# Kernel optimization log

Measured on AMD Instinct MI355X. Metric: run time of the kernel, lower is better.

Reference implementation:

```python
import jax, jax.numpy as jnp
import numpy as np

BATCH, SEQ, EMBED, HIDDEN, VOCAB = 32, 64, 512, 512, 32000

def setup_inputs() -> dict:
    key = jax.random.key(0)
    ks = jax.random.split(key, 11)
    s = lambda k, shape, scale: jax.random.normal(k, shape, dtype=jnp.float32) * scale
    return {
        "features": s(ks[0], (BATCH, HIDDEN), 1.0),
        "captions": jax.random.randint(ks[1], (BATCH, SEQ), 0, VOCAB),
        "embedding": s(ks[2], (VOCAB, EMBED), 1.0),
        "Wz_w": s(ks[3], (HIDDEN, EMBED + HIDDEN), 0.03),
        "Wz_b": s(ks[4], (HIDDEN,), 0.03),
        "Wr_w": s(ks[5], (HIDDEN, EMBED + HIDDEN), 0.03),
        "Wr_b": s(ks[6], (HIDDEN,), 0.03),
        "Wh_w": s(ks[7], (HIDDEN, EMBED + HIDDEN), 0.03),
        "Wh_b": s(ks[8], (HIDDEN,), 0.03),
        "fc_w": s(ks[9], (VOCAB, HIDDEN), 0.03),
        "fc_b": s(ks[10], (VOCAB,), 0.03),
    }

def reference(features, captions, embedding, Wz_w, Wz_b, Wr_w, Wr_b, Wh_w, Wh_b, fc_w, fc_b):
    # embeddings: [B, T, E] -> scan over time with xs [T, B, E]
    emb = embedding[captions]                      # [B, T, E]
    xs = jnp.swapaxes(emb, 0, 1)                   # [T, B, E]

    def step(h, x_t):
        comb = jnp.concatenate([x_t, h], axis=1)                   # [B, E+H]
        z = jax.nn.sigmoid(comb @ Wz_w.T + Wz_b)                   # update gate
        r = jax.nn.sigmoid(comb @ Wr_w.T + Wr_b)                   # reset gate
        comb_r = jnp.concatenate([x_t, r * h], axis=1)
        h_tilde = jnp.tanh(comb_r @ Wh_w.T + Wh_b)
        h_new = (1.0 - z) * h + z * h_tilde
        return h_new, h_new

    _, hs = jax.lax.scan(step, features, xs)       # hs: [T, B, H]
    hs = jnp.swapaxes(hs, 0, 1)                    # [B, T, H]
    # output projection done once over all timesteps (same math as per-step fc_out)
    logits = jnp.einsum('bth,vh->btv', hs, fc_w) + fc_b  # [B, T, V]
    return logits
```

## Files before the change

kernel.cpp:

```cpp
#include <hip/hip_runtime.h>
#include <hip/hip_bf16.h>

typedef __bf16 bf16;
typedef __bf16 bf16x8 __attribute__((ext_vector_type(8)));
typedef float f32x4 __attribute__((ext_vector_type(4)));
typedef unsigned int u32x4 __attribute__((ext_vector_type(4)));

#define B_SZ 32
#define T_SZ 64
#define H_SZ 512
#define V_SZ 32000
#define NWG_REC 8

__device__ __forceinline__ float sigmoidf_(float v) { return 1.0f / (1.0f + expf(-v)); }

__device__ __forceinline__ bf16x8 cvt8(const float* __restrict__ p) {
  float4 a = *(const float4*)p;
  float4 b = *(const float4*)(p + 4);
  bf16x8 o;
  o[0] = (bf16)a.x; o[1] = (bf16)a.y; o[2] = (bf16)a.z; o[3] = (bf16)a.w;
  o[4] = (bf16)b.x; o[5] = (bf16)b.y; o[6] = (bf16)b.z; o[7] = (bf16)b.w;
  return o;
}

__device__ __forceinline__ u32x4 llc_load8(const bf16* p) {
  u32x4 r;
  asm volatile("global_load_dwordx4 %0, %1, off sc0 sc1" : "=v"(r) : "v"(p));
  return r;
}
__device__ __forceinline__ void llc_store_bf16(bf16* p, float v) {
  unsigned short us = __builtin_bit_cast(unsigned short, (bf16)v);
  unsigned int w = us;
  asm volatile("global_store_short %0, %1, off sc0 sc1" :: "v"(p), "v"(w) : "memory");
}

__global__ void init_k(const float* __restrict__ feat, bf16* __restrict__ h_g,
                       int* __restrict__ ctr) {
  int i = blockIdx.x * blockDim.x + threadIdx.x;
  if (i < B_SZ * H_SZ) h_g[i] = (bf16)feat[i];
  if (i == 0) *ctr = 0;
}

__global__ void cvt_fcw(const float* __restrict__ src, bf16* __restrict__ dst, long n) {
  long i = (long)(blockIdx.x * blockDim.x + threadIdx.x) * 8;
  if (i < n) *(bf16x8*)(dst + i) = cvt8(src + i);
}

__global__ void cvt_wh(const float* __restrict__ Wz, const float* __restrict__ Wr,
                       const float* __restrict__ Wh, bf16* __restrict__ dst) {
  int i = blockIdx.x * blockDim.x + threadIdx.x;
  int w = i >> 15;
  int rem = i & 32767;
  int n = rem >> 6;
  int k8 = (rem & 63) * 8;
  const float* W = (w == 0) ? Wz : (w == 1) ? Wr : Wh;
  *(bf16x8*)(dst + (long)w * 262144 + n * 512 + k8) = cvt8(W + (long)n * 1024 + 512 + k8);
}

template<int AMODE, bool BF32>
__global__ __launch_bounds__(256) void gemm_bt(
    const void* __restrict__ Av,
    const int* __restrict__ caps, const float* __restrict__ emb,
    const void* __restrict__ Bv, int ldb,
    const float* __restrict__ bias,
    float* __restrict__ C, long ldc,
    int K, int mtiles)
{
  __shared__ __align__(16) bf16 lA[128 * 32];
  __shared__ __align__(16) bf16 lB[128 * 32];
  const int tid  = threadIdx.x;
  const int lane = tid & 63;
  const int l15  = lane & 15;
  const int kb8  = (lane >> 4) * 8;
  const int wid  = tid >> 6;
  const int wm   = wid >> 1, wn = wid & 1;
  const int wg   = blockIdx.x;
  const int mtile = wg % mtiles, ntile = wg / mtiles;
  const int m0 = mtile * 128, n0 = ntile * 128;

  f32x4 acc[4][4] = {};

  for (int k0 = 0; k0 < K; k0 += 32) {
    #pragma unroll
    for (int j = 0; j < 2; ++j) {
      int c = j * 256 + tid;
      int row = c >> 2;
      int kc = (c & 3) * 8;
      bf16x8 av;
      if (AMODE == 1) av = cvt8(emb + (long)caps[m0 + row] * K + k0 + kc);
      else            av = *(const bf16x8*)((const bf16*)Av + (long)(m0 + row) * K + k0 + kc);
      *(bf16x8*)&lA[row * 32 + kc] = av;
      bf16x8 bv;
      if (BF32) bv = cvt8((const float*)Bv + (long)(n0 + row) * ldb + k0 + kc);
      else      bv = *(const bf16x8*)((const bf16*)Bv + (long)(n0 + row) * ldb + k0 + kc);
      *(bf16x8*)&lB[row * 32 + kc] = bv;
    }
    __syncthreads();
    bf16x8 af[4], bfr[4];
    #pragma unroll
    for (int mf = 0; mf < 4; ++mf)
      af[mf] = *(const bf16x8*)&lA[(wm * 64 + mf * 16 + l15) * 32 + kb8];
    #pragma unroll
    for (int nf = 0; nf < 4; ++nf)
      bfr[nf] = *(const bf16x8*)&lB[(wn * 64 + nf * 16 + l15) * 32 + kb8];
    #pragma unroll
    for (int mf = 0; mf < 4; ++mf)
      #pragma unroll
      for (int nf = 0; nf < 4; ++nf)
        acc[mf][nf] = __builtin_amdgcn_mfma_f32_16x16x32_bf16(af[mf], bfr[nf], acc[mf][nf], 0, 0, 0);
    __syncthreads();
  }

  #pragma unroll
  for (int mf = 0; mf < 4; ++mf)
    #pragma unroll
    for (int nf = 0; nf < 4; ++nf)
      #pragma unroll
      for (int r = 0; r < 4; ++r) {
        int row = m0 + wm * 64 + mf * 16 + (lane >> 4) * 4 + r;
        int col = n0 + wn * 64 + nf * 16 + l15;
        C[(long)row * ldc + col] = acc[mf][nf][r] + bias[col];
      }
}

__device__ __forceinline__ void gridbar(int* ctr, int target) {
  asm volatile("s_waitcnt vmcnt(0) lgkmcnt(0)" ::: "memory");
  __syncthreads();
  if (threadIdx.x == 0) {
    __hip_atomic_fetch_add(ctr, 1, __ATOMIC_RELAXED, __HIP_MEMORY_SCOPE_AGENT);
    while (__hip_atomic_load(ctr, __ATOMIC_RELAXED, __HIP_MEMORY_SCOPE_AGENT) < target)
      __builtin_amdgcn_s_sleep(1);
  }
  __syncthreads();
}

__global__ __launch_bounds__(512, 2) void gru_rec(
    const float* __restrict__ X,
    const bf16* __restrict__ Wzh, const bf16* __restrict__ Wrh, const bf16* __restrict__ Whh,
    const float* __restrict__ feat,
    bf16* __restrict__ h_g, bf16* __restrict__ rh_g,
    bf16* __restrict__ hs, int* ctr)
{
  __shared__ __align__(16) char ldsb[16384];
  const int tid  = threadIdx.x;
  const int u    = blockIdx.x * 8 + (tid >> 6);
  const int lane = tid & 63;
  const int l15  = lane & 15;
  const int kb   = (lane >> 4) * 8;
  const int rq   = (lane >> 4) * 4;
  const int b0   = (u >> 5) * 16;
  const int c0   = (u & 31) * 16;
  const int gcol = c0 + l15;

  u32x4 Bz[16], Br[16], Bh[16];
  #pragma unroll
  for (int kk = 0; kk < 16; ++kk) {
    Bz[kk] = *(const u32x4*)(Wzh + (long)gcol * 512 + kk * 32 + kb);
    Br[kk] = *(const u32x4*)(Wrh + (long)gcol * 512 + kk * 32 + kb);
    Bh[kk] = *(const u32x4*)(Whh + (long)gcol * 512 + kk * 32 + kb);
  }
  #pragma unroll
  for (int kk = 0; kk < 16; ++kk)
    asm volatile("" : "+v"(Bz[kk]), "+v"(Br[kk]), "+v"(Bh[kk]));

  float hprev[4];
  #pragma unroll
  for (int r = 0; r < 4; ++r) hprev[r] = feat[(b0 + rq + r) * 512 + gcol];

  int xrow[4];
  #pragma unroll
  for (int r = 0; r < 4; ++r) xrow[r] = (b0 + rq + r) * 64 * 1536;

  float xz[4], xr[4];
  #pragma unroll
  for (int r = 0; r < 4; ++r) {
    xz[r] = X[xrow[r] + gcol];
    xr[r] = X[xrow[r] + 512 + gcol];
  }

  const int srow0 = tid >> 6;
  const int soff0 = (tid * 16) ^ ((srow0 & 7) << 4);
  const int soff1 = (8192 + tid * 16) ^ ((srow0 & 7) << 4);
  const int fbase = (l15 * 1024 + (lane >> 4) * 16) ^ ((l15 & 7) << 4);

  int epoch = 0;
  for (int t = 0; t < T_SZ; ++t) {
    {
      const bf16* src = h_g + b0 * 512;
      u32x4 v0 = llc_load8(src + tid * 8);
      u32x4 v1 = llc_load8(src + 4096 + tid * 8);
      asm volatile("s_waitcnt vmcnt(0)" ::: "memory");
      __builtin_amdgcn_sched_barrier(0);
      *(u32x4*)(ldsb + soff0) = v0;
      *(u32x4*)(ldsb + soff1) = v1;
    }
    __syncthreads();
    f32x4 ze = {}, re = {};
    #pragma unroll
    for (int kk = 0; kk < 16; ++kk) {
      bf16x8 a = *(const bf16x8*)(ldsb + (fbase ^ (kk * 64)));
      ze = __builtin_amdgcn_mfma_f32_16x16x32_bf16(a, __builtin_bit_cast(bf16x8, Bz[kk]), ze, 0, 0, 0);
      re = __builtin_amdgcn_mfma_f32_16x16x32_bf16(a, __builtin_bit_cast(bf16x8, Br[kk]), re, 0, 0, 0);
    }
    float xh[4];
    #pragma unroll
    for (int r = 0; r < 4; ++r) xh[r] = X[xrow[r] + t * 1536 + 1024 + gcol];
    f32x4 zf;
    #pragma unroll
    for (int r = 0; r < 4; ++r) {
      zf[r] = sigmoidf_(ze[r] + xz[r]);
      float rv = sigmoidf_(re[r] + xr[r]);
      llc_store_bf16(rh_g + (b0 + rq + r) * 512 + gcol, rv * hprev[r]);
    }
    ++epoch;
    gridbar(ctr, NWG_REC * epoch);

    {
      const bf16* src = rh_g + b0 * 512;
      u32x4 v0 = llc_load8(src + tid * 8);
      u32x4 v1 = llc_load8(src + 4096 + tid * 8);
      asm volatile("s_waitcnt vmcnt(0)" ::: "memory");
      __builtin_amdgcn_sched_barrier(0);
      *(u32x4*)(ldsb + soff0) = v0;
      *(u32x4*)(ldsb + soff1) = v1;
    }
    __syncthreads();
    f32x4 he = {};
    #pragma unroll
    for (int kk = 0; kk < 16; ++kk) {
      bf16x8 a = *(const bf16x8*)(ldsb + (fbase ^ (kk * 64)));
      he = __builtin_amdgcn_mfma_f32_16x16x32_bf16(a, __builtin_bit_cast(bf16x8, Bh[kk]), he, 0, 0, 0);
    }
    if (t + 1 < T_SZ) {
      #pragma unroll
      for (int r = 0; r < 4; ++r) {
        xz[r] = X[xrow[r] + (t + 1) * 1536 + gcol];
        xr[r] = X[xrow[r] + (t + 1) * 1536 + 512 + gcol];
      }
    }
    #pragma unroll
    for (int r = 0; r < 4; ++r) {
      int b = b0 + rq + r;
      float ht = tanhf(he[r] + xh[r]);
      float hn = hprev[r] + zf[r] * (ht - hprev[r]);
      hprev[r] = hn;
      llc_store_bf16(h_g + b * 512 + gcol, hn);
      hs[(long)(b * 64 + t) * 512 + gcol] = (bf16)hn;
    }
    ++epoch;
    gridbar(ctr, NWG_REC * epoch);
  }
}

extern "C" void kernel_launch(void* const* d_in, const int* in_sizes, int n_in,
                              void* d_out, int out_size, void* d_ws, size_t ws_size,
                              hipStream_t stream) {
  const float* feat = (const float*)d_in[0];
  const int*   caps = (const int*)d_in[1];
  const float* emb  = (const float*)d_in[2];
  const float* Wz_w = (const float*)d_in[3];
  const float* Wz_b = (const float*)d_in[4];
  const float* Wr_w = (const float*)d_in[5];
  const float* Wr_b = (const float*)d_in[6];
  const float* Wh_w = (const float*)d_in[7];
  const float* Wh_b = (const float*)d_in[8];
  const float* fc_w = (const float*)d_in[9];
  const float* fc_b = (const float*)d_in[10];
  float* out = (float*)d_out;

  char* ws = (char*)d_ws;
  float* X_all = (float*)(ws + 0);
  bf16*  h_g   = (bf16*) (ws + 12582912);
  bf16*  rh_g  = (bf16*) (ws + 12615680);
  bf16*  hs    = (bf16*) (ws + 12648448);
  bf16*  Whp   = (bf16*) (ws + 14745600);
  int*   ctr   = (int*)  (ws + 16318464);
  bf16*  fcw16 = (bf16*) (ws + 16318528);
  const bool cvt_fc = (ws_size >= (size_t)49086600);

  init_k<<<dim3(64), dim3(256), 0, stream>>>(feat, h_g, ctr);
  cvt_wh<<<dim3(384), dim3(256), 0, stream>>>(Wz_w, Wr_w, Wh_w, Whp);
  if (cvt_fc)
    cvt_fcw<<<dim3(8000), dim3(256), 0, stream>>>(fc_w, fcw16, (long)V_SZ * H_SZ);

  gemm_bt<1, true><<<dim3(64), dim3(256), 0, stream>>>(
      nullptr, caps, emb, Wz_w, 1024, Wz_b, X_all + 0,    1536, 512, 16);
  gemm_bt<1, true><<<dim3(64), dim3(256), 0, stream>>>(
      nullptr, caps, emb, Wr_w, 1024, Wr_b, X_all + 512,  1536, 512, 16);
  gemm_bt<1, true><<<dim3(64), dim3(256), 0, stream>>>(
      nullptr, caps, emb, Wh_w, 1024, Wh_b, X_all + 1024, 1536, 512, 16);

  gru_rec<<<dim3(NWG_REC), dim3(512), 0, stream>>>(
      X_all, Whp, Whp + 262144, Whp + 524288, feat, h_g, rh_g, hs, ctr);

  if (cvt_fc)
    gemm_bt<0, false><<<dim3(4000), dim3(256), 0, stream>>>(
        hs, nullptr, nullptr, fcw16, 512, fc_b, out, 32000, 512, 16);
  else
    gemm_bt<0, true><<<dim3(4000), dim3(256), 0, stream>>>(
        hs, nullptr, nullptr, fc_w, 512, fc_b, out, 32000, 512, 16);
}
```

Baseline: 734.8 us.

## Split recurrence sync per batch group, overlap fc weight conversion, merge launches

The recurrent kernel now syncs only the 4 workgroups that share a batch group, using a per-group counter polled per wavefront instead of a grid-wide barrier. The h and rh operands are loaded straight from L2 into registers, skipping the LDS staging. Wh is streamed from memory each step instead of held in registers, which frees registers at the cost of extra loads. The fc_w bf16 conversion runs on 56 extra workgroups alongside the recurrence, and the three input-projection GEMMs and the prep kernels are each merged into a single launch. The aim is to cut barrier latency and launch count, and to hide the conversion behind the serial recurrence.

Result: slower. 1.250 ms (+70.1%).

```diff
diff --git a/kernel.cpp b/kernel.cpp
--- a/kernel.cpp
+++ b/kernel.cpp
@@ -11,6 +11,7 @@
 #define H_SZ 512
 #define V_SZ 32000
 #define NWG_REC 8
+#define NWG_TOT 64
 
 __device__ __forceinline__ float sigmoidf_(float v) { return 1.0f / (1.0f + expf(-v)); }
 
@@ -23,30 +24,32 @@
   return o;
 }
 
-__device__ __forceinline__ u32x4 llc_load8(const bf16* p) {
-  u32x4 r;
-  asm volatile("global_load_dwordx4 %0, %1, off sc0 sc1" : "=v"(r) : "v"(p));
+#define GLD(dst, base, off) \
+  asm volatile("global_load_dwordx4 %0, %1, off offset:" off " sc0 sc1" \
+               : "=v"(dst) : "v"(base))
+#define LOADALL(af, base) do { \
+  GLD(af[0],  base, "0");   GLD(af[1],  base, "64");  GLD(af[2],  base, "128"); GLD(af[3],  base, "192"); \
+  GLD(af[4],  base, "256"); GLD(af[5],  base, "320"); GLD(af[6],  base, "384"); GLD(af[7],  base, "448"); \
+  GLD(af[8],  base, "512"); GLD(af[9],  base, "576"); GLD(af[10], base, "640"); GLD(af[11], base, "704"); \
+  GLD(af[12], base, "768"); GLD(af[13], base, "832"); GLD(af[14], base, "896"); GLD(af[15], base, "960"); \
+} while (0)
+
+#define GST2(base, off, val) do { \
+  unsigned int w_ = (unsigned int)__builtin_bit_cast(unsigned short, (bf16)(val)); \
+  asm volatile("global_store_short %0, %1, off offset:" off " sc0 sc1" \
+               :: "v"(base), "v"(w_) : "memory"); \
+} while (0)
+
+__device__ __forceinline__ int llc_poll(const int* p) {
+  int r;
+  asm volatile("global_load_dword %0, %1, off sc0 sc1\n\ts_waitcnt vmcnt(0)"
+               : "=v"(r) : "v"(p) : "memory");
   return r;
 }
-__device__ __forceinline__ void llc_store_bf16(bf16* p, float v) {
-  unsigned short us = __builtin_bit_cast(unsigned short, (bf16)v);
-  unsigned int w = us;
-  asm volatile("global_store_short %0, %1, off sc0 sc1" :: "v"(p), "v"(w) : "memory");
-}
-
-__global__ void init_k(const float* __restrict__ feat, bf16* __restrict__ h_g,
-                       int* __restrict__ ctr) {
-  int i = blockIdx.x * blockDim.x + threadIdx.x;
-  if (i < B_SZ * H_SZ) h_g[i] = (bf16)feat[i];
-  if (i == 0) *ctr = 0;
-}
-
-__global__ void cvt_fcw(const float* __restrict__ src, bf16* __restrict__ dst, long n) {
-  long i = (long)(blockIdx.x * blockDim.x + threadIdx.x) * 8;
-  if (i < n) *(bf16x8*)(dst + i) = cvt8(src + i);
-}
-
-__global__ void cvt_wh(const float* __restrict__ Wz, const float* __restrict__ Wr,
+
+__global__ void prep_k(const float* __restrict__ feat, bf16* __restrict__ h_g,
+                       int* __restrict__ ctr,
+                       const float* __restrict__ Wz, const float* __restrict__ Wr,
                        const float* __restrict__ Wh, bf16* __restrict__ dst) {
   int i = blockIdx.x * blockDim.x + threadIdx.x;
   int w = i >> 15;
@@ -55,16 +58,16 @@
   int k8 = (rem & 63) * 8;
   const float* W = (w == 0) ? Wz : (w == 1) ? Wr : Wh;
   *(bf16x8*)(dst + (long)w * 262144 + n * 512 + k8) = cvt8(W + (long)n * 1024 + 512 + k8);
+  if (i < B_SZ * H_SZ) h_g[i] = (bf16)feat[i];
+  if (i == 0) { ctr[0] = 0; ctr[64] = 0; }
 }
 
 template<int AMODE, bool BF32>
 __global__ __launch_bounds__(256) void gemm_bt(
-    const void* __restrict__ Av,
-    const int* __restrict__ caps, const float* __restrict__ emb,
-    const void* __restrict__ Bv, int ldb,
-    const float* __restrict__ bias,
-    float* __restrict__ C, long ldc,
-    int K, int mtiles)
+    const void* __restrict__ Av, const int* __restrict__ caps, const float* __restrict__ emb,
+    const void* __restrict__ B0, const void* __restrict__ B1, const void* __restrict__ B2, int ldb,
+    const float* __restrict__ bias0, const float* __restrict__ bias1, const float* __restrict__ bias2,
+    float* __restrict__ C, long ldc, int K, int mtiles)
 {
   __shared__ __align__(16) bf16 lA[128 * 32];
   __shared__ __align__(16) bf16 lB[128 * 32];
@@ -78,6 +81,14 @@
   const int mtile = wg % mtiles, ntile = wg / mtiles;
   const int m0 = mtile * 128, n0 = ntile * 128;
 
+  const void* Bv; const float* bias; int nb;
+  if (AMODE == 1) {
+    int wsel = n0 >> 9;
+    Bv = wsel == 0 ? B0 : wsel == 1 ? B1 : B2;
+    bias = wsel == 0 ? bias0 : wsel == 1 ? bias1 : bias2;
+    nb = n0 & 511;
+  } else { Bv = B0; bias = bias0; nb = n0; }
+
   f32x4 acc[4][4] = {};
 
   for (int k0 = 0; k0 < K; k0 += 32) {
@@ -91,8 +102,8 @@
       else            av = *(const bf16x8*)((const bf16*)Av + (long)(m0 + row) * K + k0 + kc);
       *(bf16x8*)&lA[row * 32 + kc] = av;
       bf16x8 bv;
-      if (BF32) bv = cvt8((const float*)Bv + (long)(n0 + row) * ldb + k0 + kc);
-      else      bv = *(const bf16x8*)((const bf16*)Bv + (long)(n0 + row) * ldb + k0 + kc);
+      if (BF32) bv = cvt8((const float*)Bv + (long)(nb + row) * ldb + k0 + kc);
+      else      bv = *(const bf16x8*)((const bf16*)Bv + (long)(nb + row) * ldb + k0 + kc);
       *(bf16x8*)&lB[row * 32 + kc] = bv;
     }
     __syncthreads();
@@ -118,20 +129,9 @@
       #pragma unroll
       for (int r = 0; r < 4; ++r) {
         int row = m0 + wm * 64 + mf * 16 + (lane >> 4) * 4 + r;
-        int col = n0 + wn * 64 + nf * 16 + l15;
-        C[(long)row * ldc + col] = acc[mf][nf][r] + bias[col];
+        int lc  = wn * 64 + nf * 16 + l15;
+        C[(long)row * ldc + n0 + lc] = acc[mf][nf][r] + bias[nb + lc];
       }
-}
-
-__device__ __forceinline__ void gridbar(int* ctr, int target) {
-  asm volatile("s_waitcnt vmcnt(0) lgkmcnt(0)" ::: "memory");
-  __syncthreads();
-  if (threadIdx.x == 0) {
-    __hip_atomic_fetch_add(ctr, 1, __ATOMIC_RELAXED, __HIP_MEMORY_SCOPE_AGENT);
-    while (__hip_atomic_load(ctr, __ATOMIC_RELAXED, __HIP_MEMORY_SCOPE_AGENT) < target)
-      __builtin_amdgcn_s_sleep(1);
-  }
-  __syncthreads();
 }
 
 __global__ __launch_bounds__(512, 2) void gru_rec(
@@ -139,116 +139,127 @@
     const bf16* __restrict__ Wzh, const bf16* __restrict__ Wrh, const bf16* __restrict__ Whh,
     const float* __restrict__ feat,
     bf16* __restrict__ h_g, bf16* __restrict__ rh_g,
-    bf16* __restrict__ hs, int* ctr)
+    bf16* __restrict__ hs, int* __restrict__ ctr,
+    const float* __restrict__ fcw_src, bf16* __restrict__ fcw_dst, int do_cvt)
 {
-  __shared__ __align__(16) char ldsb[16384];
-  const int tid  = threadIdx.x;
+  const int tid = threadIdx.x;
+  if (blockIdx.x >= NWG_REC) {
+    if (do_cvt) {
+      long base = ((long)(blockIdx.x - NWG_REC) * 512 + tid) * 8;
+      const long stride = (long)(NWG_TOT - NWG_REC) * 512 * 8;
+      for (long i = base; i < (long)V_SZ * H_SZ; i += stride)
+        *(bf16x8*)(fcw_dst + i) = cvt8(fcw_src + i);
+    }
+    return;
+  }
+
+  const int lane = tid & 63;
   const int u    = blockIdx.x * 8 + (tid >> 6);
-  const int lane = tid & 63;
   const int l15  = lane & 15;
   const int kb   = (lane >> 4) * 8;
   const int rq   = (lane >> 4) * 4;
-  const int b0   = (u >> 5) * 16;
-  const int c0   = (u & 31) * 16;
-  const int gcol = c0 + l15;
-
-  u32x4 Bz[16], Br[16], Bh[16];
+  const int grp  = u >> 5;
+  const int b0   = grp * 16;
+  const int gcol = (u & 31) * 16 + l15;
+  int* mctr = ctr + grp * 64;
+
+  u32x4 Bz[16], Br[16];
   #pragma unroll
   for (int kk = 0; kk < 16; ++kk) {
     Bz[kk] = *(const u32x4*)(Wzh + (long)gcol * 512 + kk * 32 + kb);
     Br[kk] = *(const u32x4*)(Wrh + (long)gcol * 512 + kk * 32 + kb);
-    Bh[kk] = *(const u32x4*)(Whh + (long)gcol * 512 + kk * 32 + kb);
-  }
-  #pragma unroll
-  for (int kk = 0; kk < 16; ++kk)
-    asm volatile("" : "+v"(Bz[kk]), "+v"(Br[kk]), "+v"(Bh[kk]));
+  }
+  const bf16* whbase = Whh + (long)gcol * 512 + kb;
 
   float hprev[4];
   #pragma unroll
   for (int r = 0; r < 4; ++r) hprev[r] = feat[(b0 + rq + r) * 512 + gcol];
 
-  int xrow[4];
-  #pragma unroll
-  for (int r = 0; r < 4; ++r) xrow[r] = (b0 + rq + r) * 64 * 1536;
-
+  const float* xb = X + (long)(b0 + rq) * 64 * 1536 + gcol;
   float xz[4], xr[4];
   #pragma unroll
   for (int r = 0; r < 4; ++r) {
-    xz[r] = X[xrow[r] + gcol];
-    xr[r] = X[xrow[r] + 512 + gcol];
-  }
-
-  const int srow0 = tid >> 6;
-  const int soff0 = (tid * 16) ^ ((srow0 & 7) << 4);
-  const int soff1 = (8192 + tid * 16) ^ ((srow0 & 7) << 4);
-  const int fbase = (l15 * 1024 + (lane >> 4) * 16) ^ ((l15 & 7) << 4);
-
-  int epoch = 0;
+    xz[r] = xb[r * 98304];
+    xr[r] = xb[r * 98304 + 512];
+  }
+
+  const bf16* ah   = h_g  + (b0 + l15) * 512 + kb;
+  const bf16* arh  = rh_g + (b0 + l15) * 512 + kb;
+  bf16* rhst = rh_g + (b0 + rq) * 512 + gcol;
+  bf16* hst  = h_g  + (b0 + rq) * 512 + gcol;
+  bf16* hsst = hs + (long)(b0 + rq) * 64 * 512 + gcol;
+
+  int tgt = 0;
   for (int t = 0; t < T_SZ; ++t) {
+    u32x4 af[16];
+    LOADALL(af, ah);
+    asm volatile("s_waitcnt vmcnt(0)" ::: "memory");
+    __builtin_amdgcn_sched_barrier(0);
+    f32x4 ze = {}, re = {};
+    #pragma unroll
+    for (int kk = 0; kk < 16; ++kk) {
+      bf16x8 a = __builtin_bit_cast(bf16x8, af[kk]);
+      ze = __builtin_amdgcn_mfma_f32_16x16x32_bf16(a, __builtin_bit_cast(bf16x8, Bz[kk]), ze, 0, 0, 0);
+      re = __builtin_amdgcn_mfma_f32_16x16x32_bf16(a, __builtin_bit_cast(bf16x8, Br[kk]), re, 0, 0, 0);
+    }
+    f32x4 zf;
     {
-      const bf16* src = h_g + b0 * 512;
-      u32x4 v0 = llc_load8(src + tid * 8);
-      u32x4 v1 = llc_load8(src + 4096 + tid * 8);
+      float r0 = sigmoidf_(re[0] + xr[0]) * hprev[0];
+      float r1 = sigmoidf_(re[1] + xr[1]) * hprev[1];
+      float r2 = sigmoidf_(re[2] + xr[2]) * hprev[2];
+      float r3 = sigmoidf_(re[3] + xr[3]) * hprev[3];
+      GST2(rhst, "0", r0); GST2(rhst, "1024", r1); GST2(rhst, "2048", r2); GST2(rhst, "3072", r3);
+      #pragma unroll
+      for (int r = 0; r < 4; ++r) zf[r] = sigmoidf_(ze[r] + xz[r]);
+    }
+    asm volatile("s_waitcnt vmcnt(0)" ::: "memory");
+    __builtin_amdgcn_sched_barrier(0);
+    tgt += 32;
+    if (lane == 0) __hip_atomic_fetch_add(mctr, 1, __ATOMIC_RELAXED, __HIP_MEMORY_SCOPE_AGENT);
+    __builtin_amdgcn_sched_barrier(0);
+    while (llc_poll(mctr) < tgt) __builtin_amdgcn_s_sleep(1);
+    __builtin_amdgcn_sched_barrier(0);
+
+    LOADALL(af, arh);
+    float xh[4];
+    #pragma unroll
+    for (int r = 0; r < 4; ++r) xh[r] = xb[r * 98304 + t * 1536 + 1024];
+    asm volatile("s_waitcnt vmcnt(0)" ::: "memory");
+    __builtin_amdgcn_sched_barrier(0);
+    f32x4 he = {};
+    #pragma unroll
+    for (int kk = 0; kk < 16; ++kk) {
+      u32x4 bh = *(const u32x4*)(whbase + kk * 32);
+      he = __builtin_amdgcn_mfma_f32_16x16x32_bf16(
+          __builtin_bit_cast(bf16x8, af[kk]), __builtin_bit_cast(bf16x8, bh), he, 0, 0, 0);
+    }
+    #pragma unroll
+    for (int r = 0; r < 4; ++r) {
+      float ht = tanhf(he[r] + xh[r]);
+      hprev[r] = hprev[r] + zf[r] * (ht - hprev[r]);
+    }
+    GST2(hst, "0", hprev[0]); GST2(hst, "1024", hprev[1]);
+    GST2(hst, "2048", hprev[2]); GST2(hst, "3072", hprev[3]);
+
+    if (t + 1 < T_SZ) {
       asm volatile("s_waitcnt vmcnt(0)" ::: "memory");
       __builtin_amdgcn_sched_barrier(0);
-      *(u32x4*)(ldsb + soff0) = v0;
-      *(u32x4*)(ldsb + soff1) = v1;
-    }
-    __syncthreads();
-    f32x4 ze = {}, re = {};
-    #pragma unroll
-    for (int kk = 0; kk < 16; ++kk) {
-      bf16x8 a = *(const bf16x8*)(ldsb + (fbase ^ (kk * 64)));
-      ze = __builtin_amdgcn_mfma_f32_16x16x32_bf16(a, __builtin_bit_cast(bf16x8, Bz[kk]), ze, 0, 0, 0);
-      re = __builtin_amdgcn_mfma_f32_16x16x32_bf16(a, __builtin_bit_cast(bf16x8, Br[kk]), re, 0, 0, 0);
-    }
-    float xh[4];
-    #pragma unroll
-    for (int r = 0; r < 4; ++r) xh[r] = X[xrow[r] + t * 1536 + 1024 + gcol];
-    f32x4 zf;
-    #pragma unroll
-    for (int r = 0; r < 4; ++r) {
-      zf[r] = sigmoidf_(ze[r] + xz[r]);
-      float rv = sigmoidf_(re[r] + xr[r]);
-      llc_store_bf16(rh_g + (b0 + rq + r) * 512 + gcol, rv * hprev[r]);
-    }
-    ++epoch;
-    gridbar(ctr, NWG_REC * epoch);
-
-    {
-      const bf16* src = rh_g + b0 * 512;
-      u32x4 v0 = llc_load8(src + tid * 8);
-      u32x4 v1 = llc_load8(src + 4096 + tid * 8);
-      asm volatile("s_waitcnt vmcnt(0)" ::: "memory");
+      tgt += 32;
+      if (lane == 0) __hip_atomic_fetch_add(mctr, 1, __ATOMIC_RELAXED, __HIP_MEMORY_SCOPE_AGENT);
+      #pragma unroll
+      for (int r = 0; r < 4; ++r) hsst[r * 32768 + t * 512] = (bf16)hprev[r];
+      #pragma unroll
+      for (int r = 0; r < 4; ++r) {
+        xz[r] = xb[r * 98304 + (t + 1) * 1536];
+        xr[r] = xb[r * 98304 + (t + 1) * 1536 + 512];
+      }
       __builtin_amdgcn_sched_barrier(0);
-      *(u32x4*)(ldsb + soff0) = v0;
-      *(u32x4*)(ldsb + soff1) = v1;
-    }
-    __syncthreads();
-    f32x4 he = {};
-    #pragma unroll
-    for (int kk = 0; kk < 16; ++kk) {
-      bf16x8 a = *(const bf16x8*)(ldsb + (fbase ^ (kk * 64)));
-      he = __builtin_amdgcn_mfma_f32_16x16x32_bf16(a, __builtin_bit_cast(bf16x8, Bh[kk]), he, 0, 0, 0);
-    }
-    if (t + 1 < T_SZ) {
-      #pragma unroll
-      for (int r = 0; r < 4; ++r) {
-        xz[r] = X[xrow[r] + (t + 1) * 1536 + gcol];
-        xr[r] = X[xrow[r] + (t + 1) * 1536 + 512 + gcol];
-      }
-    }
-    #pragma unroll
-    for (int r = 0; r < 4; ++r) {
-      int b = b0 + rq + r;
-      float ht = tanhf(he[r] + xh[r]);
-      float hn = hprev[r] + zf[r] * (ht - hprev[r]);
-      hprev[r] = hn;
-      llc_store_bf16(h_g + b * 512 + gcol, hn);
-      hs[(long)(b * 64 + t) * 512 + gcol] = (bf16)hn;
-    }
-    ++epoch;
-    gridbar(ctr, NWG_REC * epoch);
+      while (llc_poll(mctr) < tgt) __builtin_amdgcn_s_sleep(1);
+      __builtin_amdgcn_sched_barrier(0);
+    } else {
+      #pragma unroll
+      for (int r = 0; r < 4; ++r) hsst[r * 32768 + t * 512] = (bf16)hprev[r];
+    }
   }
 }
 
@@ -275,28 +286,25 @@
   bf16*  hs    = (bf16*) (ws + 12648448);
   bf16*  Whp   = (bf16*) (ws + 14745600);
   int*   ctr   = (int*)  (ws + 16318464);
-  bf16*  fcw16 = (bf16*) (ws + 16318528);
-  const bool cvt_fc = (ws_size >= (size_t)49086600);
-
-  init_k<<<dim3(64), dim3(256), 0, stream>>>(feat, h_g, ctr);
-  cvt_wh<<<dim3(384), dim3(256), 0, stream>>>(Wz_w, Wr_w, Wh_w, Whp);
-  if (cvt_fc)
-    cvt_fcw<<<dim3(8000), dim3(256), 0, stream>>>(fc_w, fcw16, (long)V_SZ * H_SZ);
-
-  gemm_bt<1, true><<<dim3(64), dim3(256), 0, stream>>>(
-      nullptr, caps, emb, Wz_w, 1024, Wz_b, X_all + 0,    1536, 512, 16);
-  gemm_bt<1, true><<<dim3(64), dim3(256), 0, stream>>>(
-      nullptr, caps, emb, Wr_w, 1024, Wr_b, X_all + 512,  1536, 512, 16);
-  gemm_bt<1, true><<<dim3(64), dim3(256), 0, stream>>>(
-      nullptr, caps, emb, Wh_w, 1024, Wh_b, X_all + 1024, 1536, 512, 16);
-
-  gru_rec<<<dim3(NWG_REC), dim3(512), 0, stream>>>(
-      X_all, Whp, Whp + 262144, Whp + 524288, feat, h_g, rh_g, hs, ctr);
+  bf16*  fcw16 = (bf16*) (ws + 16318976);
+  const bool cvt_fc = (ws_size >= (size_t)49087000);
+
+  prep_k<<<dim3(384), dim3(256), 0, stream>>>(feat, h_g, ctr, Wz_w, Wr_w, Wh_w, Whp);
+
+  gemm_bt<1, true><<<dim3(192), dim3(256), 0, stream>>>(
+      nullptr, caps, emb, Wz_w, Wr_w, Wh_w, 1024, Wz_b, Wr_b, Wh_b,
+      X_all, 1536, 512, 16);
+
+  gru_rec<<<dim3(NWG_TOT), dim3(512), 0, stream>>>(
+      X_all, Whp, Whp + 262144, Whp + 524288, feat, h_g, rh_g, hs, ctr,
+      fc_w, fcw16, cvt_fc ? 1 : 0);
 
   if (cvt_fc)
     gemm_bt<0, false><<<dim3(4000), dim3(256), 0, stream>>>(
-        hs, nullptr, nullptr, fcw16, 512, fc_b, out, 32000, 512, 16);
+        hs, nullptr, nullptr, fcw16, nullptr, nullptr, 512, fc_b, nullptr, nullptr,
+        out, 32000, 512, 16);
   else
     gemm_bt<0, true><<<dim3(4000), dim3(256), 0, stream>>>(
-        hs, nullptr, nullptr, fc_w, 512, fc_b, out, 32000, 512, 16);
-}
+        hs, nullptr, nullptr, fc_w, nullptr, nullptr, 512, fc_b, nullptr, nullptr,
+        out, 32000, 512, 16);
+}
```
